# Kernel tuning notes

Hardware: AMD Instinct MI355X
Metric: run time of the kernel (lower is better)

## Reference

```python
import jax, jax.numpy as jnp
import numpy as np

N_NODES = 50000
N_EDGES = 800000
D = 64        # input_nf == output_nf
HID = 64      # hidden_nf
NQ = 3        # n_qubits
NORM = 100.0  # normalization_factor, aggregation_method='sum'
MU = 0.5      # hardcoded self.mu

silu = jax.nn.silu
_Zv = jnp.array([1.0, -1.0])


def _zax(q):
    # Z eigenvalues broadcast along qubit axis q of a [N,2,2,2] statevector
    return _Zv.reshape(tuple(2 if k == q else 1 for k in range(NQ)))


def _quantum_circuit(x, alpha, beta, gamma, delta, Lam):
    """Batched 3-qubit statevector simulation of the PennyLane circuit.
    x: [N, NQ] per-node rotation inputs. Returns [N, NQ] Pauli-Z expvals."""
    N = x.shape[0]
    st = jnp.zeros((N, 2, 2, 2), jnp.complex64).at[:, 0, 0, 0].set(1.0)

    def ap(st, U, q):  # apply 2x2 gate U ([2,2] const or [N,2,2] batched) on qubit q
        st = jnp.moveaxis(st, 1 + q, 3)
        sub = 'nij,nabj->nabi' if U.ndim == 3 else 'ij,nabj->nabi'
        st = jnp.einsum(sub, U, st)
        return jnp.moveaxis(st, 3, 1 + q)

    def rz(st, theta, q):  # diagonal RZ(theta) with per-node theta [N]
        ph = jnp.exp(-0.5j * theta.astype(jnp.complex64)[:, None] * _Zv)  # [N,2]
        return st * ph.reshape((N,) + tuple(2 if k == q else 1 for k in range(NQ)))

    def ry_mat(theta):  # [N] -> [N,2,2]
        c, s = jnp.cos(theta / 2), jnp.sin(theta / 2)
        return jnp.stack([jnp.stack([c, -s], -1), jnp.stack([s, c], -1)], -2).astype(jnp.complex64)

    cb, sb = jnp.cos(beta / 2), jnp.sin(beta / 2)
    RX = jnp.stack([jnp.stack([cb + 0j, -1j * sb]), jnp.stack([-1j * sb, cb + 0j])])
    Hm = jnp.array([[1.0, 1.0], [1.0, -1.0]], jnp.complex64) / np.sqrt(2.0)

    # 1) data-encoding RY layer
    for q in range(NQ):
        st = ap(st, ry_mat(x[:, q] * alpha), q)
    # 2) coupling Hamiltonian: IsingZZ(gamma*(Lam_ij+Lam_ji)/2) on each pair (diagonal phase)
    for i in range(NQ):
        for j in range(i + 1, NQ):
            phi = gamma * (Lam[i, j] + Lam[j, i]) / 2
            st = st * jnp.exp(-0.5j * phi * (_zax(i) * _zax(j)))[None]
    # 3) kinetic RX layer
    for q in range(NQ):
        st = ap(st, RX, q)
    # 4) anharmonic layer: RZ, H, RZ, H per qubit
    for q in range(NQ):
        st = rz(st, delta * (1.0 - MU * x[:, q] ** 2), q)
        st = ap(st, Hm, q)
        st = rz(st, delta * x[:, q] ** 2, q)
        st = ap(st, Hm, q)
    # 5) final kinetic RX layer
    for q in range(NQ):
        st = ap(st, RX, q)

    probs = jnp.abs(st) ** 2  # [N,2,2,2]
    return jnp.stack([jnp.sum(probs * _zax(q)[None], axis=(1, 2, 3)) for q in range(NQ)], axis=1)


def setup_inputs() -> dict:
    key = jax.random.key(0)
    ks = jax.random.split(key, 10)
    def w(k, shape):
        return jax.random.normal(k, shape, jnp.float32) * 0.05
    h = jax.random.normal(ks[0], (N_NODES, D), jnp.float32)
    edge_index = jax.random.randint(ks[1], (2, N_EDGES), 0, N_NODES)
    Lam = jnp.full((NQ, NQ), -0.1 / (NQ - 1), jnp.float32).at[jnp.arange(NQ), jnp.arange(NQ)].set(0.1)
    return {
        'h': h, 'edge_index': edge_index,
        'eW1': w(ks[2], (2 * D, HID)), 'eb1': jnp.zeros(HID, jnp.float32),
        'eW2': w(ks[3], (HID, HID)), 'eb2': jnp.zeros(HID, jnp.float32),
        'qW1': w(ks[4], (D + HID, HID)), 'qb1': jnp.zeros(HID, jnp.float32),
        'qW2': w(ks[5], (HID, NQ)), 'qb2': jnp.zeros(NQ, jnp.float32),
        'pW1': w(ks[6], (D + HID + NQ, HID)), 'pb1': jnp.zeros(HID, jnp.float32),
        'pW2': w(ks[7], (HID, D)), 'pb2': jnp.zeros(D, jnp.float32),
        'alpha': jnp.float32(0.1 / NQ), 'beta': jnp.float32(np.pi / (4 * NQ)),
        'gamma': jnp.float32(0.1 / NQ), 'delta': jnp.float32(0.05),
        'Lambda': Lam,
    }


def reference(h, edge_index, eW1, eb1, eW2, eb2, qW1, qb1, qW2, qb2,
              pW1, pb1, pW2, pb2, alpha, beta, gamma, delta, Lambda):
    row, col = edge_index[0], edge_index[1]
    # edge model (no attention, no edge_attr, no edge_mask)
    e_in = jnp.concatenate([h[row], h[col]], axis=1)           # [E, 2D]
    mij = silu(silu(e_in @ eW1 + eb1) @ eW2 + eb2)             # [E, HID]
    # node model: scatter-sum aggregation normalized by factor ('sum' mode)
    agg = jax.ops.segment_sum(mij, row, num_segments=N_NODES) / NORM
    a = jnp.concatenate([h, agg], axis=1)                      # [N, D+HID]
    q_in = silu(a @ qW1 + qb1) @ qW2 + qb2                     # [N, NQ]
    # original detaches inputs and rebuilds outputs via torch.tensor -> no grad flow
    q_out = jax.lax.stop_gradient(
        _quantum_circuit(jax.lax.stop_gradient(q_in), alpha, beta, gamma, delta, Lambda)
    ).astype(h.dtype)
    a2 = jnp.concatenate([a, q_out], axis=1)                   # [N, 2*HID+NQ]
    out = h + (silu(a2 @ pW1 + pb1) @ pW2 + pb2)
    return out, mij
```

## Files before the change

kernel.cpp:

```cpp
#include <hip/hip_runtime.h>
#include <hip/hip_bf16.h>
#include <math.h>
#include <stdint.h>


#define N_NODES 50000
#define N_EDGES 800000
#define DIM 64
#define HID 64
#define T_EDGE (N_EDGES / 16)
#define T_NODE (N_NODES / 16)
#define EDGE_GRID 768
#define NODE_GRID 512

typedef __bf16 bf16_t;
typedef __bf16 bf16x8 __attribute__((ext_vector_type(8)));
typedef float f32x4 __attribute__((ext_vector_type(4)));

__device__ __forceinline__ float silu_f(float x) {
    return x / (1.f + __expf(-x));
}

__device__ __forceinline__ f32x4 mfma16(bf16x8 a, bf16x8 b, f32x4 c) {
    return __builtin_amdgcn_mfma_f32_16x16x32_bf16(a, b, c, 0, 0, 0);
}

__device__ __forceinline__ bf16x8 cvt8(const float* __restrict__ p) {
    f32x4 u0 = *(const f32x4*)p;
    f32x4 u1 = *(const f32x4*)(p + 4);
    bf16x8 r;
    r[0] = (bf16_t)u0[0]; r[1] = (bf16_t)u0[1]; r[2] = (bf16_t)u0[2]; r[3] = (bf16_t)u0[3];
    r[4] = (bf16_t)u1[0]; r[5] = (bf16_t)u1[1]; r[6] = (bf16_t)u1[2]; r[7] = (bf16_t)u1[3];
    return r;
}

__device__ __forceinline__ void atomic_pk_bf16(bf16_t* p, float lo, float hi) {
    union { bf16_t h2[2]; uint32_t u; } pk;
    pk.h2[0] = (bf16_t)lo; pk.h2[1] = (bf16_t)hi;
    asm volatile("global_atomic_pk_add_bf16 %0, %1, off"
                 :: "v"((uint64_t)(uintptr_t)p), "v"(pk.u) : "memory");
}

__global__ __launch_bounds__(256) void init_kernel(const float* __restrict__ h,
                                                   bf16_t* __restrict__ hb,
                                                   bf16_t* __restrict__ aggz, int n8)
{
    int i = blockIdx.x * 256 + threadIdx.x;
    if (i < n8) {
        *(bf16x8*)(hb + (size_t)i * 8) = cvt8(h + (size_t)i * 8);
        bf16x8 zz;
        #pragma unroll
        for (int j = 0; j < 8; ++j) zz[j] = (bf16_t)0.f;
        *(bf16x8*)(aggz + (size_t)i * 8) = zz;
    }
}

__global__ __launch_bounds__(512) void edge_kernel(
    const bf16_t* __restrict__ hb,
    const int* __restrict__ ei,
    const float* __restrict__ eW1, const float* __restrict__ eb1,
    const float* __restrict__ eW2, const float* __restrict__ eb2,
    float* __restrict__ mij_out,
    bf16_t* __restrict__ agg)
{
    __shared__ __align__(16) bf16_t sB1[64][136];
    __shared__ __align__(16) bf16_t sB2[64][72];
    __shared__ __align__(16) bf16_t sHid[8][16][72];
    __shared__ float sb1[64], sb2[64];

    const int tid = threadIdx.x;
    for (int idx = tid; idx < 128 * 64; idx += 512) {
        int k = idx >> 6, n = idx & 63;
        sB1[n][k] = (bf16_t)eW1[idx];
    }
    for (int idx = tid; idx < 64 * 64; idx += 512) {
        int k = idx >> 6, n = idx & 63;
        sB2[n][k] = (bf16_t)eW2[idx];
    }
    if (tid < 64) { sb1[tid] = eb1[tid]; sb2[tid] = eb2[tid]; }
    __syncthreads();

    const int l = tid & 63, wave = tid >> 6;
    const int m = l & 15, quad = l >> 4;
    const f32x4 z = {0.f, 0.f, 0.f, 0.f};

    for (int t = blockIdx.x * 8 + wave; t < T_EDGE; t += EDGE_GRID * 8) {
        const int e0 = t * 16;
        int ev = ei[e0 + m + ((quad & 1) ? N_EDGES : 0)];
        const int nrow = __shfl(ev, m);
        const int ncol = __shfl(ev, 16 + m);
        const bf16_t* ra = hb + (size_t)nrow * DIM;
        const bf16_t* rb = hb + (size_t)ncol * DIM;

        f32x4 acc[4] = {z, z, z, z};
        #pragma unroll
        for (int ks = 0; ks < 4; ++ks) {
            const int k0 = ks * 32 + quad * 8;
            bf16x8 a = *(const bf16x8*)((k0 < 64) ? (ra + k0) : (rb + (k0 - 64)));
            #pragma unroll
            for (int nt = 0; nt < 4; ++nt)
                acc[nt] = mfma16(a, *(const bf16x8*)&sB1[nt * 16 + m][k0], acc[nt]);
        }
        #pragma unroll
        for (int nt = 0; nt < 4; ++nt)
            #pragma unroll
            for (int rr = 0; rr < 4; ++rr) {
                int row = quad * 4 + rr, col = nt * 16 + m;
                sHid[wave][row][col] = (bf16_t)silu_f(acc[nt][rr] + sb1[col]);
            }

        f32x4 acc2[4] = {z, z, z, z};
        #pragma unroll
        for (int ks = 0; ks < 2; ++ks) {
            const int k0 = ks * 32 + quad * 8;
            bf16x8 a = *(const bf16x8*)&sHid[wave][m][k0];
            #pragma unroll
            for (int nt = 0; nt < 4; ++nt)
                acc2[nt] = mfma16(a, *(const bf16x8*)&sB2[nt * 16 + m][k0], acc2[nt]);
        }

        int dstrow[4];
        #pragma unroll
        for (int rr = 0; rr < 4; ++rr) dstrow[rr] = __shfl(nrow, quad * 4 + rr);

        #pragma unroll
        for (int nt = 0; nt < 4; ++nt) {
            #pragma unroll
            for (int rr = 0; rr < 4; ++rr) {
                int row = quad * 4 + rr;
                int col = nt * 16 + m;
                float v = silu_f(acc2[nt][rr] + sb2[col]);
                __builtin_nontemporal_store(v, &mij_out[(size_t)(e0 + row) * HID + col]);
                float vh = __shfl_xor(v, 1);
                if ((l & 1) == 0) {
                    atomic_pk_bf16(agg + (size_t)dstrow[rr] * HID + col, v, vh);
                }
            }
        }
    }
}

__global__ __launch_bounds__(512) void node_kernel(
    const float* __restrict__ h, const bf16_t* __restrict__ aggb,
    const float* __restrict__ qW1, const float* __restrict__ qb1,
    const float* __restrict__ qW2, const float* __restrict__ qb2,
    const float* __restrict__ pW1, const float* __restrict__ pb1,
    const float* __restrict__ pW2, const float* __restrict__ pb2,
    const float* __restrict__ al_p, const float* __restrict__ be_p,
    const float* __restrict__ ga_p, const float* __restrict__ de_p,
    const float* __restrict__ lam_p,
    float* __restrict__ out)
{
    __shared__ __align__(16) bf16_t sQ1[64][136];
    __shared__ __align__(16) bf16_t sP1[64][136];
    __shared__ __align__(16) bf16_t sP2[64][72];
    __shared__ __align__(16) bf16_t sQ2b[16][72];
    __shared__ __align__(16) bf16_t sHid[8][16][72];
    __shared__ float sQio[8][16][4];
    __shared__ __align__(16) float sqb1[64];
    __shared__ __align__(16) float spb1[64];
    __shared__ __align__(16) float spb2[64];
    __shared__ float sqb2[4];

    const int tid = threadIdx.x;
    for (int idx = tid; idx < 128 * 64; idx += 512) {
        int k = idx >> 6, n = idx & 63;
        float w = qW1[idx];
        sQ1[n][k] = (bf16_t)(k < 64 ? w : w * 0.01f);
    }
    for (int idx = tid; idx < 131 * 64; idx += 512) {
        int k = idx >> 6, n = idx & 63;
        float w = pW1[idx];
        sP1[n][k] = (bf16_t)((k >= 64 && k < 128) ? w * 0.01f : w);
    }
    for (int idx = tid; idx < 5 * 64; idx += 512) {
        int k = 131 + (idx >> 6), n = idx & 63;
        sP1[n][k] = (bf16_t)0.f;
    }
    for (int idx = tid; idx < 64 * 64; idx += 512) {
        int k = idx >> 6, n = idx & 63;
        sP2[n][k] = (bf16_t)pW2[idx];
    }
    for (int idx = tid; idx < 16 * 72; idx += 512) {
        int c = idx / 72, k = idx - c * 72;
        sQ2b[c][k] = (bf16_t)((c < 3 && k < 64) ? qW2[k * 3 + c] : 0.f);
    }
    if (tid < 64) { sqb1[tid] = qb1[tid]; spb1[tid] = pb1[tid]; spb2[tid] = pb2[tid]; }
    if (tid < 3) sqb2[tid] = qb2[tid];
    __syncthreads();

    const int lane = tid & 63, wave = tid >> 6;
    const int m = lane & 15, quad = lane >> 4;
    const float al = al_p[0], be = be_p[0];
    const float ga = ga_p[0], de = de_p[0];
    const float phi01 = ga * (lam_p[1] + lam_p[3]) * 0.5f;
    const float phi02 = ga * (lam_p[2] + lam_p[6]) * 0.5f;
    const float phi12 = ga * (lam_p[5] + lam_p[7]) * 0.5f;
    const float cbg = __cosf(0.5f * be), sbg = __sinf(0.5f * be);
    const f32x4 z = {0.f, 0.f, 0.f, 0.f};

    for (int t = blockIdx.x * 8 + wave; t < T_NODE; t += NODE_GRID * 8) {
        const int n0 = t * 16;
        const float* hrow = h + (size_t)(n0 + m) * DIM;
        const bf16_t* grow = aggb + (size_t)(n0 + m) * HID;

        bf16x8 afr[4];
        #pragma unroll
        for (int ks = 0; ks < 4; ++ks) {
            const int k0 = ks * 32 + quad * 8;
            afr[ks] = (k0 < 64) ? cvt8(hrow + k0)
                                : *(const bf16x8*)(grow + (k0 - 64));
        }

        f32x4 acc[4] = {z, z, z, z};
        #pragma unroll
        for (int ks = 0; ks < 4; ++ks) {
            const int k0 = ks * 32 + quad * 8;
            #pragma unroll
            for (int nt = 0; nt < 4; ++nt)
                acc[nt] = mfma16(afr[ks], *(const bf16x8*)&sQ1[nt * 16 + m][k0], acc[nt]);
        }
        #pragma unroll
        for (int nt = 0; nt < 4; ++nt)
            #pragma unroll
            for (int rr = 0; rr < 4; ++rr) {
                int row = quad * 4 + rr, col = nt * 16 + m;
                sHid[wave][row][col] = (bf16_t)silu_f(acc[nt][rr] + sqb1[col]);
            }

        f32x4 aq = z;
        #pragma unroll
        for (int ks = 0; ks < 2; ++ks) {
            const int k0 = ks * 32 + quad * 8;
            bf16x8 a = *(const bf16x8*)&sHid[wave][m][k0];
            bf16x8 b = *(const bf16x8*)&sQ2b[m][k0];
            aq = mfma16(a, b, aq);
        }
        if (m < 3) {
            #pragma unroll
            for (int rr = 0; rr < 4; ++rr)
                sQio[wave][quad * 4 + rr][m] = aq[rr] + sqb2[m];
        }

        if (lane < 16) {
            float qin[3];
            qin[0] = sQio[wave][lane][0];
            qin[1] = sQio[wave][lane][1];
            qin[2] = sQio[wave][lane][2];
            float re[8], im[8];
            float cc[3], ssn[3];
            #pragma unroll
            for (int q = 0; q < 3; ++q) {
                float th = 0.5f * qin[q] * al;
                cc[q] = __cosf(th); ssn[q] = __sinf(th);
            }
            #pragma unroll
            for (int i = 0; i < 8; ++i) {
                float v0 = (i & 4) ? ssn[0] : cc[0];
                float v1 = (i & 2) ? ssn[1] : cc[1];
                float v2 = (i & 1) ? ssn[2] : cc[2];
                re[i] = v0 * v1 * v2; im[i] = 0.f;
            }
            #pragma unroll
            for (int i = 0; i < 8; ++i) {
                float z0 = (i & 4) ? -1.f : 1.f;
                float z1 = (i & 2) ? -1.f : 1.f;
                float z2 = (i & 1) ? -1.f : 1.f;
                float th = -0.5f * (phi01 * z0 * z1 + phi02 * z0 * z2 + phi12 * z1 * z2);
                float ct = __cosf(th), st = __sinf(th);
                float r = re[i], iM = im[i];
                re[i] = r * ct - iM * st;
                im[i] = r * st + iM * ct;
            }
            auto rx = [&](int q) {
                int msk = 4 >> q;
                #pragma unroll
                for (int i = 0; i < 8; ++i) {
                    if (i & msk) continue;
                    int j = i | msk;
                    float r0 = re[i], i0 = im[i], r1 = re[j], i1 = im[j];
                    re[i] = cbg * r0 + sbg * i1;
                    im[i] = cbg * i0 - sbg * r1;
                    re[j] = sbg * i0 + cbg * r1;
                    im[j] = -sbg * r0 + cbg * i1;
                }
            };
            auto hgate = [&](int q) {
                const float inv = 0.70710678f;
                int msk = 4 >> q;
                #pragma unroll
                for (int i = 0; i < 8; ++i) {
                    if (i & msk) continue;
                    int j = i | msk;
                    float r0 = re[i], i0 = im[i], r1 = re[j], i1 = im[j];
                    re[i] = (r0 + r1) * inv; im[i] = (i0 + i1) * inv;
                    re[j] = (r0 - r1) * inv; im[j] = (i0 - i1) * inv;
                }
            };
            auto rzg = [&](int q, float th) {
                int msk = 4 >> q;
                float c = __cosf(0.5f * th), s = __sinf(0.5f * th);
                #pragma unroll
                for (int i = 0; i < 8; ++i) {
                    float sg = (i & msk) ? s : -s;
                    float r = re[i], iM = im[i];
                    re[i] = r * c - iM * sg;
                    im[i] = r * sg + iM * c;
                }
            };
            rx(0); rx(1); rx(2);
            #pragma unroll
            for (int q = 0; q < 3; ++q) {
                float x = qin[q];
                rzg(q, de * (1.f - 0.5f * x * x));
                hgate(q);
                rzg(q, de * x * x);
                hgate(q);
            }
            rx(0); rx(1); rx(2);
            float e0v = 0.f, e1v = 0.f, e2v = 0.f;
            #pragma unroll
            for (int i = 0; i < 8; ++i) {
                float p = re[i] * re[i] + im[i] * im[i];
                e0v += (i & 4) ? -p : p;
                e1v += (i & 2) ? -p : p;
                e2v += (i & 1) ? -p : p;
            }
            sQio[wave][lane][0] = e0v;
            sQio[wave][lane][1] = e1v;
            sQio[wave][lane][2] = e2v;
        }

        f32x4 acc2[4] = {z, z, z, z};
        #pragma unroll
        for (int ks = 0; ks < 4; ++ks) {
            const int k0 = ks * 32 + quad * 8;
            #pragma unroll
            for (int nt = 0; nt < 4; ++nt)
                acc2[nt] = mfma16(afr[ks], *(const bf16x8*)&sP1[nt * 16 + m][k0], acc2[nt]);
        }
        {
            bf16x8 a, bz;
            #pragma unroll
            for (int j = 0; j < 8; ++j) { a[j] = (bf16_t)0.f; bz[j] = (bf16_t)0.f; }
            if (quad == 0) {
                a[0] = (bf16_t)sQio[wave][m][0];
                a[1] = (bf16_t)sQio[wave][m][1];
                a[2] = (bf16_t)sQio[wave][m][2];
            }
            #pragma unroll
            for (int nt = 0; nt < 4; ++nt) {
                bf16x8 b = bz;
                if (quad == 0) b = *(const bf16x8*)&sP1[nt * 16 + m][128];
                acc2[nt] = mfma16(a, b, acc2[nt]);
            }
        }
        #pragma unroll
        for (int nt = 0; nt < 4; ++nt)
            #pragma unroll
            for (int rr = 0; rr < 4; ++rr) {
                int row = quad * 4 + rr, col = nt * 16 + m;
                sHid[wave][row][col] = (bf16_t)silu_f(acc2[nt][rr] + spb1[col]);
            }

        f32x4 acc3[4] = {z, z, z, z};
        #pragma unroll
        for (int ks = 0; ks < 2; ++ks) {
            const int k0 = ks * 32 + quad * 8;
            bf16x8 hfrag = *(const bf16x8*)&sHid[wave][m][k0];
            #pragma unroll
            for (int nt = 0; nt < 4; ++nt)
                acc3[nt] = mfma16(*(const bf16x8*)&sP2[nt * 16 + m][k0], hfrag, acc3[nt]);
        }
        {
            const int node = n0 + m;
            const float* hr = h + (size_t)node * DIM;
            float* orow = out + (size_t)node * DIM;
            #pragma unroll
            for (int nt = 0; nt < 4; ++nt) {
                const int c0 = nt * 16 + quad * 4;
                f32x4 hv = *(const f32x4*)(hr + c0);
                f32x4 bias = *(const f32x4*)&spb2[c0];
                f32x4 v;
                #pragma unroll
                for (int rr = 0; rr < 4; ++rr) v[rr] = acc3[nt][rr] + bias[rr] + hv[rr];
                __builtin_nontemporal_store(v, (f32x4*)(orow + c0));
            }
        }
    }
}

extern "C" void kernel_launch(void* const* d_in, const int* in_sizes, int n_in,
                              void* d_out, int out_size, void* d_ws, size_t ws_size,
                              hipStream_t stream)
{
    const float* h   = (const float*)d_in[0];
    const int* ei    = (const int*)d_in[1];
    const float* eW1 = (const float*)d_in[2];
    const float* eb1 = (const float*)d_in[3];
    const float* eW2 = (const float*)d_in[4];
    const float* eb2 = (const float*)d_in[5];
    const float* qW1 = (const float*)d_in[6];
    const float* qb1 = (const float*)d_in[7];
    const float* qW2 = (const float*)d_in[8];
    const float* qb2 = (const float*)d_in[9];
    const float* pW1 = (const float*)d_in[10];
    const float* pb1 = (const float*)d_in[11];
    const float* pW2 = (const float*)d_in[12];
    const float* pb2 = (const float*)d_in[13];
    const float* al  = (const float*)d_in[14];
    const float* be  = (const float*)d_in[15];
    const float* ga  = (const float*)d_in[16];
    const float* de  = (const float*)d_in[17];
    const float* lam = (const float*)d_in[18];

    float* out = (float*)d_out;
    float* mij = out + (size_t)N_NODES * DIM;
    bf16_t* aggb = (bf16_t*)d_ws;
    bf16_t* hb   = aggb + (size_t)N_NODES * HID;

    const int n8 = (N_NODES * DIM) / 8;

    init_kernel<<<(n8 + 255) / 256, 256, 0, stream>>>(h, hb, aggb, n8);
    edge_kernel<<<EDGE_GRID, 512, 0, stream>>>(hb, ei, eW1, eb1, eW2, eb2, mij, aggb);
    node_kernel<<<NODE_GRID, 512, 0, stream>>>(h, aggb, qW1, qb1, qW2, qb2,
                                               pW1, pb1, pW2, pb2,
                                               al, be, ga, de, lam, out);
}
```

Baseline: 444.6 us.

## Software-pipeline edge gathers by prefetching next tile's node rows

Restructures the persistent edge loop so that the next tile's edge indices and gathered h rows are loaded into registers while the current tile's MLP and atomics run. The aim is to hide global gather latency behind MFMA and epilogue work. It also replaces the division in silu with a hardware reciprocal. The cost is higher register pressure, which could reduce occupancy.

```diff
diff --git a/kernel.cpp b/kernel.cpp
--- a/kernel.cpp
+++ b/kernel.cpp
@@ -18,7 +18,7 @@
 typedef float f32x4 __attribute__((ext_vector_type(4)));
 
 __device__ __forceinline__ float silu_f(float x) {
-    return x / (1.f + __expf(-x));
+    return x * __builtin_amdgcn_rcpf(1.f + __expf(-x));
 }
 
 __device__ __forceinline__ f32x4 mfma16(bf16x8 a, bf16x8 b, f32x4 c) {
@@ -82,24 +82,41 @@
 
     const int l = tid & 63, wave = tid >> 6;
     const int m = l & 15, quad = l >> 4;
+    const int eisel = m + ((quad & 1) ? N_EDGES : 0);
     const f32x4 z = {0.f, 0.f, 0.f, 0.f};
 
-    for (int t = blockIdx.x * 8 + wave; t < T_EDGE; t += EDGE_GRID * 8) {
-        const int e0 = t * 16;
-        int ev = ei[e0 + m + ((quad & 1) ? N_EDGES : 0)];
-        const int nrow = __shfl(ev, m);
-        const int ncol = __shfl(ev, 16 + m);
+    int t = blockIdx.x * 8 + wave;
+    if (t >= T_EDGE) return;
+
+    int ev = ei[t * 16 + eisel];
+    int nrow = __shfl(ev, m);
+    int ncol = __shfl(ev, 16 + m);
+    bf16x8 a_cur[4];
+    {
         const bf16_t* ra = hb + (size_t)nrow * DIM;
         const bf16_t* rb = hb + (size_t)ncol * DIM;
+        #pragma unroll
+        for (int ks = 0; ks < 4; ++ks) {
+            const int k0 = ks * 32 + quad * 8;
+            a_cur[ks] = *(const bf16x8*)((k0 < 64) ? (ra + k0) : (rb + (k0 - 64)));
+        }
+    }
+
+    while (true) {
+        const int e0 = t * 16;
+        const int tn = t + EDGE_GRID * 8;
+        const bool has_next = (tn < T_EDGE);
+
+        int evn = 0;
+        if (has_next) evn = ei[tn * 16 + eisel];
 
         f32x4 acc[4] = {z, z, z, z};
         #pragma unroll
         for (int ks = 0; ks < 4; ++ks) {
             const int k0 = ks * 32 + quad * 8;
-            bf16x8 a = *(const bf16x8*)((k0 < 64) ? (ra + k0) : (rb + (k0 - 64)));
             #pragma unroll
             for (int nt = 0; nt < 4; ++nt)
-                acc[nt] = mfma16(a, *(const bf16x8*)&sB1[nt * 16 + m][k0], acc[nt]);
+                acc[nt] = mfma16(a_cur[ks], *(const bf16x8*)&sB1[nt * 16 + m][k0], acc[nt]);
         }
         #pragma unroll
         for (int nt = 0; nt < 4; ++nt)
@@ -108,6 +125,20 @@
                 int row = quad * 4 + rr, col = nt * 16 + m;
                 sHid[wave][row][col] = (bf16_t)silu_f(acc[nt][rr] + sb1[col]);
             }
+
+        int nrow_n = 0, ncol_n = 0;
+        bf16x8 a_nxt[4];
+        if (has_next) {
+            nrow_n = __shfl(evn, m);
+            ncol_n = __shfl(evn, 16 + m);
+            const bf16_t* ra = hb + (size_t)nrow_n * DIM;
+            const bf16_t* rb = hb + (size_t)ncol_n * DIM;
+            #pragma unroll
+            for (int ks = 0; ks < 4; ++ks) {
+                const int k0 = ks * 32 + quad * 8;
+                a_nxt[ks] = *(const bf16x8*)((k0 < 64) ? (ra + k0) : (rb + (k0 - 64)));
+            }
+        }
 
         f32x4 acc2[4] = {z, z, z, z};
         #pragma unroll
@@ -137,6 +168,12 @@
                 }
             }
         }
+
+        if (!has_next) break;
+        t = tn;
+        nrow = nrow_n; ncol = ncol_n;
+        #pragma unroll
+        for (int ks = 0; ks < 4; ++ks) a_cur[ks] = a_nxt[ks];
     }
 }
 
```

Measured after the change: 439.6 us. No clear change (-1.1%).
